# Kernel optimization log

Hardware: AMD Instinct MI355X
Metric: run time of the kernel (lower is better)

## Reference

```python
import jax, jax.numpy as jnp
import numpy as np

N0, N1, N2, N3 = 600000, 100000, 10000, 1000
E0, E1, E2 = 1000000, 100000, 10000
DIN, DH, DOUT = 128, 256, 47


def _glorot(k, fan_in, fan_out):
    s = np.sqrt(2.0 / (fan_in + fan_out)).astype(np.float32)
    return jax.random.normal(k, (fan_in, fan_out), jnp.float32) * s


def setup_inputs() -> dict:
    key = jax.random.key(0)
    ks = jax.random.split(key, 13)
    return {
        "x": jax.random.normal(ks[0], (N0, DIN), jnp.float32),
        "src0": jax.random.randint(ks[1], (E0,), 0, N0, jnp.int32),
        "dst0": jax.random.randint(ks[2], (E0,), 0, N1, jnp.int32),
        "src1": jax.random.randint(ks[3], (E1,), 0, N1, jnp.int32),
        "dst1": jax.random.randint(ks[4], (E1,), 0, N2, jnp.int32),
        "src2": jax.random.randint(ks[5], (E2,), 0, N2, jnp.int32),
        "dst2": jax.random.randint(ks[6], (E2,), 0, N3, jnp.int32),
        "Wl0": _glorot(ks[7], DIN, DH), "Wr0": _glorot(ks[8], DIN, DH),
        "b0": jnp.zeros((DH,), jnp.float32),
        "Wl1": _glorot(ks[9], DH, DH), "Wr1": _glorot(ks[10], DH, DH),
        "b1": jnp.zeros((DH,), jnp.float32),
        "Wl2": _glorot(ks[11], DH, DOUT), "Wr2": _glorot(ks[12], DH, DOUT),
        "b2": jnp.zeros((DOUT,), jnp.float32),
        "size1": N1, "size2": N2, "size3": N3,
    }


def _sage_conv(x, src, dst, n_tgt, Wl, Wr, b):
    # PyG SAGEConv (mean aggr, root_weight=True, bias in lin_l) on a bipartite
    # sampled subgraph: x_src = x (all frontier nodes), x_tgt = x[:n_tgt].
    msgs = x[src]                                   # [E, Din] gather
    agg = jax.ops.segment_sum(msgs, dst, num_segments=n_tgt)
    cnt = jax.ops.segment_sum(jnp.ones((dst.shape[0],), x.dtype), dst,
                              num_segments=n_tgt)
    mean = agg / jnp.maximum(cnt, 1.0)[:, None]     # [n_tgt, Din]
    return mean @ Wl + b + x[:n_tgt] @ Wr           # [n_tgt, Dout]


def reference(x, src0, dst0, src1, dst1, src2, dst2,
              Wl0, Wr0, b0, Wl1, Wr1, b1, Wl2, Wr2, b2,
              size1, size2, size3):
    # layer 0
    h = jax.nn.relu(_sage_conv(x, src0, dst0, size1, Wl0, Wr0, b0))
    # dropout(p=0.5) is identity in eval mode
    # layer 1
    h = jax.nn.relu(_sage_conv(h, src1, dst1, size2, Wl1, Wr1, b1))
    # layer 2 (no relu/dropout)
    h = _sage_conv(h, src2, dst2, size3, Wl2, Wr2, b2)
    return jax.nn.log_softmax(h, axis=-1)           # [size3, out_channels]
```

## Files before the change

### kernel.cpp

```cpp
#include <hip/hip_runtime.h>
#include <hip/hip_bf16.h>
#include <cstdint>
#include <cstddef>
#include <cmath>

#define N0C 600000
#define N1C 100000
#define N2C 10000
#define N3C 1000
#define E0C 1000000
#define E1C 100000
#define E2C 10000

typedef unsigned short u16;
typedef unsigned int u32;
typedef __attribute__((ext_vector_type(8))) short bf16x8;
typedef __attribute__((ext_vector_type(4))) float f32x4;

__device__ __forceinline__ u16 f2b(float x) {
  u32 u = __builtin_bit_cast(u32, x);
  u32 r = (u + 0x7fffu + ((u >> 16) & 1u)) >> 16;
  return (u16)r;
}
__device__ __forceinline__ u16 f2b_hw(float x) {
  __hip_bfloat16 h = __float2bfloat16(x);
  u16 r;
  __builtin_memcpy(&r, &h, 2);
  return r;
}
__device__ __forceinline__ float b2f(u16 h) {
  u32 u = ((u32)h) << 16;
  return __builtin_bit_cast(float, u);
}

__global__ __launch_bounds__(256) void hist3(
    const int* __restrict__ d0, const int* __restrict__ d1,
    const int* __restrict__ d2, int* __restrict__ c0, int* __restrict__ c1,
    int* __restrict__ c2) {
  int i = blockIdx.x * blockDim.x + threadIdx.x;
  if (i < E0C) atomicAdd(&c0[d0[i]], 1);
  else if (i < E0C + E1C) atomicAdd(&c1[d1[i - E0C]], 1);
  else if (i < E0C + E1C + E2C) atomicAdd(&c2[d2[i - E0C - E1C]], 1);
}

__global__ __launch_bounds__(256) void scan_block3(
    int* __restrict__ c0, int* __restrict__ c1, int* __restrict__ c2,
    int* __restrict__ p0, int* __restrict__ p1, int* __restrict__ p2) {
  __shared__ int sdata[256];
  const int b = blockIdx.x;
  int* data; int n; int* partials; int lb;
  if (b < 98)       { data = c0; n = N1C; partials = p0; lb = b; }
  else if (b < 108) { data = c1; n = N2C; partials = p1; lb = b - 98; }
  else              { data = c2; n = N3C; partials = p2; lb = b - 108; }
  const int t = threadIdx.x;
  const int idx = lb * 1024 + t * 4;
  int v[4];
  int sum = 0;
#pragma unroll
  for (int k = 0; k < 4; k++) {
    int x = (idx + k < n) ? data[idx + k] : 0;
    v[k] = x; sum += x;
  }
  sdata[t] = sum;
  __syncthreads();
  for (int off = 1; off < 256; off <<= 1) {
    int x = (t >= off) ? sdata[t - off] : 0;
    __syncthreads();
    sdata[t] += x;
    __syncthreads();
  }
  int run = (t > 0) ? sdata[t - 1] : 0;
#pragma unroll
  for (int k = 0; k < 4; k++) {
    run += v[k];
    if (idx + k < n) data[idx + k] = run;
  }
  if (t == 255) partials[lb] = sdata[255];
}

__global__ __launch_bounds__(128) void scan_partials3(
    int* __restrict__ p0, int* __restrict__ p1, int* __restrict__ p2) {
  __shared__ int sdata[128];
  int* p; int nb;
  if (blockIdx.x == 0)      { p = p0; nb = 98; }
  else if (blockIdx.x == 1) { p = p1; nb = 10; }
  else                      { p = p2; nb = 1; }
  const int t = threadIdx.x;
  sdata[t] = (t < nb) ? p[t] : 0;
  __syncthreads();
  for (int off = 1; off < 128; off <<= 1) {
    int x = (t >= off) ? sdata[t - off] : 0;
    __syncthreads();
    sdata[t] += x;
    __syncthreads();
  }
  int ex = (t > 0) ? sdata[t - 1] : 0;
  if (t < nb) p[t] = ex;
}

__global__ __launch_bounds__(256) void addoff3(
    const int* __restrict__ c0, const int* __restrict__ c1,
    const int* __restrict__ c2, const int* __restrict__ p0,
    const int* __restrict__ p1, const int* __restrict__ p2,
    int* __restrict__ o0, int* __restrict__ o1, int* __restrict__ o2) {
  int i = blockIdx.x * blockDim.x + threadIdx.x;
  if (i < N1C) {
    o0[i + 1] = c0[i] + p0[i >> 10];
    if (i == 0) o0[0] = 0;
  } else if (i < N1C + N2C) {
    int j = i - N1C;
    o1[j + 1] = c1[j] + p1[j >> 10];
    if (j == 0) o1[0] = 0;
  } else if (i < N1C + N2C + N3C) {
    int j = i - N1C - N2C;
    o2[j + 1] = c2[j] + p2[j >> 10];
    if (j == 0) o2[0] = 0;
  }
}

__global__ __launch_bounds__(256) void fill3(
    const int* __restrict__ s0, const int* __restrict__ d0,
    const int* __restrict__ s1, const int* __restrict__ d1,
    const int* __restrict__ s2, const int* __restrict__ d2,
    const int* __restrict__ o0, const int* __restrict__ o1,
    const int* __restrict__ o2, int* __restrict__ u0, int* __restrict__ u1,
    int* __restrict__ u2, int* __restrict__ e0, int* __restrict__ e1,
    int* __restrict__ e2) {
  int i = blockIdx.x * blockDim.x + threadIdx.x;
  if (i < E0C) {
    int d = d0[i]; int p = atomicAdd(&u0[d], 1); e0[o0[d] + p] = s0[i];
  } else if (i < E0C + E1C) {
    int j = i - E0C;
    int d = d1[j]; int p = atomicAdd(&u1[d], 1); e1[o1[d] + p] = s1[j];
  } else if (i < E0C + E1C + E2C) {
    int j = i - E0C - E1C;
    int d = d2[j]; int p = atomicAdd(&u2[d], 1); e2[o2[d] + p] = s2[j];
  }
}

__global__ __launch_bounds__(256) void cvt_wt2(
    const float* __restrict__ Wl0, const float* __restrict__ Wr0,
    const float* __restrict__ Wl1, const float* __restrict__ Wr1,
    u16* __restrict__ Wt0, u16* __restrict__ Wt1) {
  int idx = blockIdx.x * blockDim.x + threadIdx.x;
  if (idx < 256 * 256) {
    int n = idx >> 8, k = idx & 255;
    float v = (k < 128) ? Wl0[(size_t)k * 256 + n] : Wr0[(size_t)(k - 128) * 256 + n];
    Wt0[idx] = f2b(v);
  } else if (idx < 256 * 256 + 256 * 512) {
    int j = idx - 256 * 256;
    int n = j >> 9, k = j & 511;
    float v = (k < 256) ? Wl1[(size_t)k * 256 + n] : Wr1[(size_t)(k - 256) * 256 + n];
    Wt1[j] = f2b(v);
  }
}

__global__ __launch_bounds__(256) void gather128_f32(
    const float* __restrict__ X, const int* __restrict__ off,
    const int* __restrict__ esrc, int Nt, u16* __restrict__ mean) {
  int w = (blockIdx.x * blockDim.x + threadIdx.x) >> 6;
  int lane = threadIdx.x & 63;
  if (w >= Nt) return;
  int s = off[w], e = off[w + 1];
  float a0 = 0.f, a1 = 0.f;
  int j = s;
  for (; j + 3 < e; j += 4) {
    float2 r0 = *(const float2*)(X + (size_t)esrc[j + 0] * 128 + lane * 2);
    float2 r1 = *(const float2*)(X + (size_t)esrc[j + 1] * 128 + lane * 2);
    float2 r2 = *(const float2*)(X + (size_t)esrc[j + 2] * 128 + lane * 2);
    float2 r3 = *(const float2*)(X + (size_t)esrc[j + 3] * 128 + lane * 2);
    a0 += r0.x + r1.x + r2.x + r3.x;
    a1 += r0.y + r1.y + r2.y + r3.y;
  }
  for (; j < e; j++) {
    float2 r = *(const float2*)(X + (size_t)esrc[j] * 128 + lane * 2);
    a0 += r.x;
    a1 += r.y;
  }
  float inv = 1.0f / fmaxf((float)(e - s), 1.0f);
  u32 p = ((u32)f2b(a1 * inv) << 16) | (u32)f2b(a0 * inv);
  ((u32*)(mean + (size_t)w * 128))[lane] = p;
}

__global__ __launch_bounds__(256) void gather256_bf16(
    const u16* __restrict__ X, const int* __restrict__ off,
    const int* __restrict__ esrc, int Nt, u16* __restrict__ mean) {
  int w = (blockIdx.x * blockDim.x + threadIdx.x) >> 6;
  int lane = threadIdx.x & 63;
  if (w >= Nt) return;
  int s = off[w], e = off[w + 1];
  float a0 = 0.f, a1 = 0.f, a2 = 0.f, a3 = 0.f;
  int j = s;
  for (; j + 3 < e; j += 4) {
    ushort4 v0 = *(const ushort4*)(X + (size_t)esrc[j + 0] * 256 + lane * 4);
    ushort4 v1 = *(const ushort4*)(X + (size_t)esrc[j + 1] * 256 + lane * 4);
    ushort4 v2 = *(const ushort4*)(X + (size_t)esrc[j + 2] * 256 + lane * 4);
    ushort4 v3 = *(const ushort4*)(X + (size_t)esrc[j + 3] * 256 + lane * 4);
    a0 += b2f(v0.x) + b2f(v1.x) + b2f(v2.x) + b2f(v3.x);
    a1 += b2f(v0.y) + b2f(v1.y) + b2f(v2.y) + b2f(v3.y);
    a2 += b2f(v0.z) + b2f(v1.z) + b2f(v2.z) + b2f(v3.z);
    a3 += b2f(v0.w) + b2f(v1.w) + b2f(v2.w) + b2f(v3.w);
  }
  for (; j < e; j++) {
    ushort4 v0 = *(const ushort4*)(X + (size_t)esrc[j] * 256 + lane * 4);
    a0 += b2f(v0.x); a1 += b2f(v0.y); a2 += b2f(v0.z); a3 += b2f(v0.w);
  }
  float inv = 1.0f / fmaxf((float)(e - s), 1.0f);
  ushort4 o;
  o.x = f2b(a0 * inv); o.y = f2b(a1 * inv); o.z = f2b(a2 * inv); o.w = f2b(a3 * inv);
  *(ushort4*)(mean + (size_t)w * 256 + lane * 4) = o;
}

__global__ __launch_bounds__(256) void gemm_mfma(
    const u16* __restrict__ A1, const u16* __restrict__ A2, int Kh,
    const u16* __restrict__ Wt, const float* __restrict__ bias,
    u16* __restrict__ C, int M, int do_relu) {
  const int tid = threadIdx.x;
  const int wave = tid >> 6, lane = tid & 63;
  const int lr = lane & 15, quad = lane >> 4;
  const int wr = wave >> 1, wc = wave & 1;
  const int rowBase = blockIdx.x * 128 + wr * 64;
  const int colBase = blockIdx.y * 128 + wc * 64;
  const int Ktot = 2 * Kh;

  f32x4 acc[4][4] = {};

  size_t aoff[4];
#pragma unroll
  for (int mt = 0; mt < 4; mt++) {
    int r = rowBase + mt * 16 + lr;
    if (r >= M) r = M - 1;
    aoff[mt] = (size_t)r * Kh;
  }
  const u16* wrow[4];
  float bs[4];
#pragma unroll
  for (int nt = 0; nt < 4; nt++) {
    int n = colBase + nt * 16 + lr;
    wrow[nt] = Wt + (size_t)n * Ktot;
    bs[nt] = bias[n];
  }

#pragma unroll
  for (int half = 0; half < 2; half++) {
    const u16* Asrc = half ? A2 : A1;
    const int kb = half * Kh;
    for (int kt = 0; kt < Kh; kt += 32) {
      bf16x8 af[4], bfr[4];
#pragma unroll
      for (int mt = 0; mt < 4; mt++)
        af[mt] = *(const bf16x8*)(Asrc + aoff[mt] + kt + quad * 8);
#pragma unroll
      for (int nt = 0; nt < 4; nt++)
        bfr[nt] = *(const bf16x8*)(wrow[nt] + kb + kt + quad * 8);
#pragma unroll
      for (int mt = 0; mt < 4; mt++)
#pragma unroll
        for (int nt = 0; nt < 4; nt++)
          acc[mt][nt] = __builtin_amdgcn_mfma_f32_16x16x32_bf16(
              af[mt], bfr[nt], acc[mt][nt], 0, 0, 0);
    }
  }

#pragma unroll
  for (int mt = 0; mt < 4; mt++) {
#pragma unroll
    for (int reg = 0; reg < 4; reg++) {
      int row = rowBase + mt * 16 + quad * 4 + reg;
      if (row < M) {
#pragma unroll
        for (int nt = 0; nt < 4; nt++) {
          float v = acc[mt][nt][reg] + bs[nt];
          if (do_relu) v = fmaxf(v, 0.f);
          C[(size_t)row * 256 + colBase + nt * 16 + lr] = f2b(v);
        }
      }
    }
  }
}

__global__ __launch_bounds__(256) void gemm_mfma_l0(
    const u16* __restrict__ A1, const float* __restrict__ A2,
    const u16* __restrict__ Wt, const float* __restrict__ bias,
    u16* __restrict__ C, int M) {
  const int tid = threadIdx.x;
  const int wave = tid >> 6, lane = tid & 63;
  const int lr = lane & 15, quad = lane >> 4;
  const int wr = wave >> 1, wc = wave & 1;
  const int rowBase = blockIdx.x * 128 + wr * 64;
  const int colBase = blockIdx.y * 128 + wc * 64;

  f32x4 acc[4][4] = {};

  int rrow[4];
#pragma unroll
  for (int mt = 0; mt < 4; mt++) {
    int r = rowBase + mt * 16 + lr;
    if (r >= M) r = M - 1;
    rrow[mt] = r;
  }
  const u16* wrow[4];
  float bs[4];
#pragma unroll
  for (int nt = 0; nt < 4; nt++) {
    int n = colBase + nt * 16 + lr;
    wrow[nt] = Wt + (size_t)n * 256;
    bs[nt] = bias[n];
  }

  for (int kt = 0; kt < 128; kt += 32) {
    bf16x8 af[4], bfr[4];
#pragma unroll
    for (int mt = 0; mt < 4; mt++)
      af[mt] = *(const bf16x8*)(A1 + (size_t)rrow[mt] * 128 + kt + quad * 8);
#pragma unroll
    for (int nt = 0; nt < 4; nt++)
      bfr[nt] = *(const bf16x8*)(wrow[nt] + kt + quad * 8);
#pragma unroll
    for (int mt = 0; mt < 4; mt++)
#pragma unroll
      for (int nt = 0; nt < 4; nt++)
        acc[mt][nt] = __builtin_amdgcn_mfma_f32_16x16x32_bf16(
            af[mt], bfr[nt], acc[mt][nt], 0, 0, 0);
  }
  for (int kt = 0; kt < 128; kt += 32) {
    bf16x8 af[4], bfr[4];
#pragma unroll
    for (int mt = 0; mt < 4; mt++) {
      const float* s = A2 + (size_t)rrow[mt] * 128 + kt + quad * 8;
      float4 v0 = *(const float4*)s;
      float4 v1 = *(const float4*)(s + 4);
      bf16x8 t;
      t[0] = (short)f2b_hw(v0.x); t[1] = (short)f2b_hw(v0.y);
      t[2] = (short)f2b_hw(v0.z); t[3] = (short)f2b_hw(v0.w);
      t[4] = (short)f2b_hw(v1.x); t[5] = (short)f2b_hw(v1.y);
      t[6] = (short)f2b_hw(v1.z); t[7] = (short)f2b_hw(v1.w);
      af[mt] = t;
    }
#pragma unroll
    for (int nt = 0; nt < 4; nt++)
      bfr[nt] = *(const bf16x8*)(wrow[nt] + 128 + kt + quad * 8);
#pragma unroll
    for (int mt = 0; mt < 4; mt++)
#pragma unroll
      for (int nt = 0; nt < 4; nt++)
        acc[mt][nt] = __builtin_amdgcn_mfma_f32_16x16x32_bf16(
            af[mt], bfr[nt], acc[mt][nt], 0, 0, 0);
  }

#pragma unroll
  for (int mt = 0; mt < 4; mt++) {
#pragma unroll
    for (int reg = 0; reg < 4; reg++) {
      int row = rowBase + mt * 16 + quad * 4 + reg;
      if (row < M) {
#pragma unroll
        for (int nt = 0; nt < 4; nt++) {
          float v = fmaxf(acc[mt][nt][reg] + bs[nt], 0.f);
          C[(size_t)row * 256 + colBase + nt * 16 + lr] = f2b(v);
        }
      }
    }
  }
}

__global__ __launch_bounds__(64) void layer2_lsm(
    const u16* __restrict__ mean2, const u16* __restrict__ h2,
    const float* __restrict__ Wl2, const float* __restrict__ Wr2,
    const float* __restrict__ b2, float* __restrict__ out) {
  __shared__ float arow[512];
  const int i = blockIdx.x;
  const int lane = threadIdx.x;
  for (int t = lane; t < 256; t += 64) {
    arow[t] = b2f(mean2[(size_t)i * 256 + t]);
    arow[256 + t] = b2f(h2[(size_t)i * 256 + t]);
  }
  __syncthreads();
  float acc = 0.0f;
  if (lane < 47) {
    acc = b2[lane];
#pragma unroll 4
    for (int k = 0; k < 256; k++) acc += arow[k] * Wl2[k * 47 + lane];
#pragma unroll 4
    for (int k = 0; k < 256; k++) acc += arow[256 + k] * Wr2[k * 47 + lane];
  }
  float v = (lane < 47) ? acc : -INFINITY;
#pragma unroll
  for (int off = 32; off >= 1; off >>= 1) v = fmaxf(v, __shfl_xor(v, off, 64));
  float e = (lane < 47) ? expf(acc - v) : 0.0f;
  float s = e;
#pragma unroll
  for (int off = 32; off >= 1; off >>= 1) s += __shfl_xor(s, off, 64);
  if (lane < 47) out[(size_t)i * 47 + lane] = acc - v - logf(s);
}

extern "C" void kernel_launch(void* const* d_in, const int* in_sizes, int n_in,
                              void* d_out, int out_size, void* d_ws, size_t ws_size,
                              hipStream_t stream) {
  (void)in_sizes; (void)n_in; (void)out_size; (void)ws_size;
  const float* x   = (const float*)d_in[0];
  const int* src0  = (const int*)d_in[1];
  const int* dst0  = (const int*)d_in[2];
  const int* src1  = (const int*)d_in[3];
  const int* dst1  = (const int*)d_in[4];
  const int* src2  = (const int*)d_in[5];
  const int* dst2  = (const int*)d_in[6];
  const float* Wl0 = (const float*)d_in[7];
  const float* Wr0 = (const float*)d_in[8];
  const float* b0  = (const float*)d_in[9];
  const float* Wl1 = (const float*)d_in[10];
  const float* Wr1 = (const float*)d_in[11];
  const float* b1  = (const float*)d_in[12];
  const float* Wl2 = (const float*)d_in[13];
  const float* Wr2 = (const float*)d_in[14];
  const float* b2  = (const float*)d_in[15];

  char* p = (char*)d_ws;
  u16* mean0 = (u16*)p; p += (size_t)N1C * 128 * 2;
  u16* h1    = (u16*)p; p += (size_t)N1C * 256 * 2;
  u16* mean1 = (u16*)p; p += (size_t)N2C * 256 * 2;
  u16* h2    = (u16*)p; p += (size_t)N2C * 256 * 2;
  u16* mean2 = (u16*)p; p += (size_t)N3C * 256 * 2;
  u16* Wt0   = (u16*)p; p += (size_t)256 * 256 * 2;
  u16* Wt1   = (u16*)p; p += (size_t)256 * 512 * 2;
  int* cnt0  = (int*)p;
  int* cur0  = cnt0 + 100000;
  int* cnt1  = cur0 + 100000;
  int* cur1  = cnt1 + 10000;
  int* cnt2  = cur1 + 10000;
  int* cur2  = cnt2 + 1000;
  int* off0  = cur2 + 1000 + 48;
  int* off1  = off0 + 100096;
  int* off2  = off1 + 10112;
  int* part0 = off2 + 1088;
  int* part1 = part0 + 128;
  int* part2 = part1 + 128;
  int* esrc0 = part2 + 128;
  int* esrc1 = esrc0 + 1000000;
  int* esrc2 = esrc1 + 100000;
  float* out = (float*)d_out;

  hipMemsetAsync(cnt0, 0, (size_t)222000 * 4, stream);
  hist3<<<(E0C + E1C + E2C + 255) / 256, 256, 0, stream>>>(
      dst0, dst1, dst2, cnt0, cnt1, cnt2);
  scan_block3<<<109, 256, 0, stream>>>(cnt0, cnt1, cnt2, part0, part1, part2);
  scan_partials3<<<3, 128, 0, stream>>>(part0, part1, part2);
  addoff3<<<(N1C + N2C + N3C + 255) / 256, 256, 0, stream>>>(
      cnt0, cnt1, cnt2, part0, part1, part2, off0, off1, off2);
  fill3<<<(E0C + E1C + E2C + 255) / 256, 256, 0, stream>>>(
      src0, dst0, src1, dst1, src2, dst2, off0, off1, off2,
      cur0, cur1, cur2, esrc0, esrc1, esrc2);

  cvt_wt2<<<(256 * 256 + 256 * 512 + 255) / 256, 256, 0, stream>>>(
      Wl0, Wr0, Wl1, Wr1, Wt0, Wt1);

  gather128_f32<<<N1C / 4, 256, 0, stream>>>(x, off0, esrc0, N1C, mean0);
  gemm_mfma_l0<<<dim3(782, 2), 256, 0, stream>>>(mean0, x, Wt0, b0, h1, N1C);

  gather256_bf16<<<N2C / 4, 256, 0, stream>>>(h1, off1, esrc1, N2C, mean1);
  gemm_mfma<<<dim3(79, 2), 256, 0, stream>>>(mean1, h1, 256, Wt1, b1, h2, N2C, 1);

  gather256_bf16<<<N3C / 4, 256, 0, stream>>>(h2, off2, esrc2, N3C, mean2);
  layer2_lsm<<<N3C, 64, 0, stream>>>(mean2, h2, Wl2, Wr2, b2, out);
}
```

Baseline: 745.3 us.

## Fuse layer-0 gather into GEMM via LDS and fuse layer-2 gather with output

```diff
diff --git a/kernel.cpp b/kernel.cpp
--- a/kernel.cpp
+++ b/kernel.cpp
@@ -153,33 +153,6 @@
     float v = (k < 256) ? Wl1[(size_t)k * 256 + n] : Wr1[(size_t)(k - 256) * 256 + n];
     Wt1[j] = f2b(v);
   }
-}
-
-__global__ __launch_bounds__(256) void gather128_f32(
-    const float* __restrict__ X, const int* __restrict__ off,
-    const int* __restrict__ esrc, int Nt, u16* __restrict__ mean) {
-  int w = (blockIdx.x * blockDim.x + threadIdx.x) >> 6;
-  int lane = threadIdx.x & 63;
-  if (w >= Nt) return;
-  int s = off[w], e = off[w + 1];
-  float a0 = 0.f, a1 = 0.f;
-  int j = s;
-  for (; j + 3 < e; j += 4) {
-    float2 r0 = *(const float2*)(X + (size_t)esrc[j + 0] * 128 + lane * 2);
-    float2 r1 = *(const float2*)(X + (size_t)esrc[j + 1] * 128 + lane * 2);
-    float2 r2 = *(const float2*)(X + (size_t)esrc[j + 2] * 128 + lane * 2);
-    float2 r3 = *(const float2*)(X + (size_t)esrc[j + 3] * 128 + lane * 2);
-    a0 += r0.x + r1.x + r2.x + r3.x;
-    a1 += r0.y + r1.y + r2.y + r3.y;
-  }
-  for (; j < e; j++) {
-    float2 r = *(const float2*)(X + (size_t)esrc[j] * 128 + lane * 2);
-    a0 += r.x;
-    a1 += r.y;
-  }
-  float inv = 1.0f / fmaxf((float)(e - s), 1.0f);
-  u32 p = ((u32)f2b(a1 * inv) << 16) | (u32)f2b(a0 * inv);
-  ((u32*)(mean + (size_t)w * 128))[lane] = p;
 }
 
 __global__ __launch_bounds__(256) void gather256_bf16(
@@ -211,91 +184,54 @@
   *(ushort4*)(mean + (size_t)w * 256 + lane * 4) = o;
 }
 
-__global__ __launch_bounds__(256) void gemm_mfma(
-    const u16* __restrict__ A1, const u16* __restrict__ A2, int Kh,
-    const u16* __restrict__ Wt, const float* __restrict__ bias,
-    u16* __restrict__ C, int M, int do_relu) {
+__global__ __launch_bounds__(512) void l0_fused(
+    const float* __restrict__ x, const int* __restrict__ off,
+    const int* __restrict__ esrc, const u16* __restrict__ Wt,
+    const float* __restrict__ bias, u16* __restrict__ C, int M) {
+  __shared__ u16 Al[128 * 128];
   const int tid = threadIdx.x;
   const int wave = tid >> 6, lane = tid & 63;
+  const int rowBlk = blockIdx.x * 128;
+
+  for (int i = 0; i < 16; i++) {
+    const int lrow = wave * 16 + i;
+    const int node = rowBlk + lrow;
+    float a0 = 0.f, a1 = 0.f;
+    float inv = 0.f;
+    if (node < M) {
+      int s = off[node], e = off[node + 1];
+      int j = s;
+      for (; j + 3 < e; j += 4) {
+        float2 r0 = *(const float2*)(x + (size_t)esrc[j + 0] * 128 + lane * 2);
+        float2 r1 = *(const float2*)(x + (size_t)esrc[j + 1] * 128 + lane * 2);
+        float2 r2 = *(const float2*)(x + (size_t)esrc[j + 2] * 128 + lane * 2);
+        float2 r3 = *(const float2*)(x + (size_t)esrc[j + 3] * 128 + lane * 2);
+        a0 += r0.x + r1.x + r2.x + r3.x;
+        a1 += r0.y + r1.y + r2.y + r3.y;
+      }
+      for (; j < e; j++) {
+        float2 r = *(const float2*)(x + (size_t)esrc[j] * 128 + lane * 2);
+        a0 += r.x; a1 += r.y;
+      }
+      inv = 1.0f / fmaxf((float)(e - s), 1.0f);
+    }
+    u32 pck = ((u32)f2b(a1 * inv) << 16) | (u32)f2b(a0 * inv);
+    int pc = (lane >> 2) ^ (lrow & 7);
+    ((u32*)Al)[lrow * 64 + pc * 4 + (lane & 3)] = pck;
+  }
+  __syncthreads();
+
   const int lr = lane & 15, quad = lane >> 4;
-  const int wr = wave >> 1, wc = wave & 1;
-  const int rowBase = blockIdx.x * 128 + wr * 64;
-  const int colBase = blockIdx.y * 128 + wc * 64;
-  const int Ktot = 2 * Kh;
+  const int wr = wave >> 2, wc = wave & 3;
+  const int colBase = wc * 64;
 
   f32x4 acc[4][4] = {};
 
-  size_t aoff[4];
+  int lrw[4], rrow[4];
 #pragma unroll
   for (int mt = 0; mt < 4; mt++) {
-    int r = rowBase + mt * 16 + lr;
-    if (r >= M) r = M - 1;
-    aoff[mt] = (size_t)r * Kh;
-  }
-  const u16* wrow[4];
-  float bs[4];
-#pragma unroll
-  for (int nt = 0; nt < 4; nt++) {
-    int n = colBase + nt * 16 + lr;
-    wrow[nt] = Wt + (size_t)n * Ktot;
-    bs[nt] = bias[n];
-  }
-
-#pragma unroll
-  for (int half = 0; half < 2; half++) {
-    const u16* Asrc = half ? A2 : A1;
-    const int kb = half * Kh;
-    for (int kt = 0; kt < Kh; kt += 32) {
-      bf16x8 af[4], bfr[4];
-#pragma unroll
-      for (int mt = 0; mt < 4; mt++)
-        af[mt] = *(const bf16x8*)(Asrc + aoff[mt] + kt + quad * 8);
-#pragma unroll
-      for (int nt = 0; nt < 4; nt++)
-        bfr[nt] = *(const bf16x8*)(wrow[nt] + kb + kt + quad * 8);
-#pragma unroll
-      for (int mt = 0; mt < 4; mt++)
-#pragma unroll
-        for (int nt = 0; nt < 4; nt++)
-          acc[mt][nt] = __builtin_amdgcn_mfma_f32_16x16x32_bf16(
-              af[mt], bfr[nt], acc[mt][nt], 0, 0, 0);
-    }
-  }
-
-#pragma unroll
-  for (int mt = 0; mt < 4; mt++) {
-#pragma unroll
-    for (int reg = 0; reg < 4; reg++) {
-      int row = rowBase + mt * 16 + quad * 4 + reg;
-      if (row < M) {
-#pragma unroll
-        for (int nt = 0; nt < 4; nt++) {
-          float v = acc[mt][nt][reg] + bs[nt];
-          if (do_relu) v = fmaxf(v, 0.f);
-          C[(size_t)row * 256 + colBase + nt * 16 + lr] = f2b(v);
-        }
-      }
-    }
-  }
-}
-
-__global__ __launch_bounds__(256) void gemm_mfma_l0(
-    const u16* __restrict__ A1, const float* __restrict__ A2,
-    const u16* __restrict__ Wt, const float* __restrict__ bias,
-    u16* __restrict__ C, int M) {
-  const int tid = threadIdx.x;
-  const int wave = tid >> 6, lane = tid & 63;
-  const int lr = lane & 15, quad = lane >> 4;
-  const int wr = wave >> 1, wc = wave & 1;
-  const int rowBase = blockIdx.x * 128 + wr * 64;
-  const int colBase = blockIdx.y * 128 + wc * 64;
-
-  f32x4 acc[4][4] = {};
-
-  int rrow[4];
-#pragma unroll
-  for (int mt = 0; mt < 4; mt++) {
-    int r = rowBase + mt * 16 + lr;
+    lrw[mt] = wr * 64 + mt * 16 + lr;
+    int r = rowBlk + lrw[mt];
     if (r >= M) r = M - 1;
     rrow[mt] = r;
   }
@@ -308,11 +244,15 @@
     bs[nt] = bias[n];
   }
 
+#pragma unroll
   for (int kt = 0; kt < 128; kt += 32) {
     bf16x8 af[4], bfr[4];
 #pragma unroll
-    for (int mt = 0; mt < 4; mt++)
-      af[mt] = *(const bf16x8*)(A1 + (size_t)rrow[mt] * 128 + kt + quad * 8);
+    for (int mt = 0; mt < 4; mt++) {
+      int r = lrw[mt];
+      int pc = ((kt >> 3) + quad) ^ (r & 7);
+      af[mt] = *(const bf16x8*)(Al + r * 128 + pc * 8);
+    }
 #pragma unroll
     for (int nt = 0; nt < 4; nt++)
       bfr[nt] = *(const bf16x8*)(wrow[nt] + kt + quad * 8);
@@ -323,11 +263,12 @@
         acc[mt][nt] = __builtin_amdgcn_mfma_f32_16x16x32_bf16(
             af[mt], bfr[nt], acc[mt][nt], 0, 0, 0);
   }
+#pragma unroll
   for (int kt = 0; kt < 128; kt += 32) {
     bf16x8 af[4], bfr[4];
 #pragma unroll
     for (int mt = 0; mt < 4; mt++) {
-      const float* s = A2 + (size_t)rrow[mt] * 128 + kt + quad * 8;
+      const float* s = x + (size_t)rrow[mt] * 128 + kt + quad * 8;
       float4 v0 = *(const float4*)s;
       float4 v1 = *(const float4*)(s + 4);
       bf16x8 t;
@@ -352,7 +293,7 @@
   for (int mt = 0; mt < 4; mt++) {
 #pragma unroll
     for (int reg = 0; reg < 4; reg++) {
-      int row = rowBase + mt * 16 + quad * 4 + reg;
+      int row = rowBlk + wr * 64 + mt * 16 + quad * 4 + reg;
       if (row < M) {
 #pragma unroll
         for (int nt = 0; nt < 4; nt++) {
@@ -364,18 +305,112 @@
   }
 }
 
-__global__ __launch_bounds__(64) void layer2_lsm(
-    const u16* __restrict__ mean2, const u16* __restrict__ h2,
-    const float* __restrict__ Wl2, const float* __restrict__ Wr2,
-    const float* __restrict__ b2, float* __restrict__ out) {
+__global__ __launch_bounds__(512) void gemm_mfma1(
+    const u16* __restrict__ A1, const u16* __restrict__ A2, int Kh,
+    const u16* __restrict__ Wt, const float* __restrict__ bias,
+    u16* __restrict__ C, int M, int do_relu) {
+  const int tid = threadIdx.x;
+  const int wave = tid >> 6, lane = tid & 63;
+  const int lr = lane & 15, quad = lane >> 4;
+  const int wr = wave >> 2, wc = wave & 3;
+  const int rowBase = blockIdx.x * 128 + wr * 64;
+  const int colBase = wc * 64;
+  const int Ktot = 2 * Kh;
+
+  f32x4 acc[4][4] = {};
+
+  size_t aoff[4];
+#pragma unroll
+  for (int mt = 0; mt < 4; mt++) {
+    int r = rowBase + mt * 16 + lr;
+    if (r >= M) r = M - 1;
+    aoff[mt] = (size_t)r * Kh;
+  }
+  const u16* wrow[4];
+  float bs[4];
+#pragma unroll
+  for (int nt = 0; nt < 4; nt++) {
+    int n = colBase + nt * 16 + lr;
+    wrow[nt] = Wt + (size_t)n * Ktot;
+    bs[nt] = bias[n];
+  }
+
+#pragma unroll
+  for (int half = 0; half < 2; half++) {
+    const u16* Asrc = half ? A2 : A1;
+    const int kb = half * Kh;
+    for (int kt = 0; kt < Kh; kt += 32) {
+      bf16x8 af[4], bfr[4];
+#pragma unroll
+      for (int mt = 0; mt < 4; mt++)
+        af[mt] = *(const bf16x8*)(Asrc + aoff[mt] + kt + quad * 8);
+#pragma unroll
+      for (int nt = 0; nt < 4; nt++)
+        bfr[nt] = *(const bf16x8*)(wrow[nt] + kb + kt + quad * 8);
+#pragma unroll
+      for (int mt = 0; mt < 4; mt++)
+#pragma unroll
+        for (int nt = 0; nt < 4; nt++)
+          acc[mt][nt] = __builtin_amdgcn_mfma_f32_16x16x32_bf16(
+              af[mt], bfr[nt], acc[mt][nt], 0, 0, 0);
+    }
+  }
+
+#pragma unroll
+  for (int mt = 0; mt < 4; mt++) {
+#pragma unroll
+    for (int reg = 0; reg < 4; reg++) {
+      int row = rowBase + mt * 16 + quad * 4 + reg;
+      if (row < M) {
+#pragma unroll
+        for (int nt = 0; nt < 4; nt++) {
+          float v = acc[mt][nt][reg] + bs[nt];
+          if (do_relu) v = fmaxf(v, 0.f);
+          C[(size_t)row * 256 + colBase + nt * 16 + lr] = f2b(v);
+        }
+      }
+    }
+  }
+}
+
+__global__ __launch_bounds__(64) void l2_fused(
+    const u16* __restrict__ h2, const int* __restrict__ off,
+    const int* __restrict__ esrc, const float* __restrict__ Wl2,
+    const float* __restrict__ Wr2, const float* __restrict__ b2,
+    float* __restrict__ out) {
   __shared__ float arow[512];
   const int i = blockIdx.x;
   const int lane = threadIdx.x;
-  for (int t = lane; t < 256; t += 64) {
-    arow[t] = b2f(mean2[(size_t)i * 256 + t]);
-    arow[256 + t] = b2f(h2[(size_t)i * 256 + t]);
-  }
+
+  int s = off[i], e = off[i + 1];
+  float a0 = 0.f, a1 = 0.f, a2 = 0.f, a3 = 0.f;
+  int j = s;
+  for (; j + 3 < e; j += 4) {
+    ushort4 v0 = *(const ushort4*)(h2 + (size_t)esrc[j + 0] * 256 + lane * 4);
+    ushort4 v1 = *(const ushort4*)(h2 + (size_t)esrc[j + 1] * 256 + lane * 4);
+    ushort4 v2 = *(const ushort4*)(h2 + (size_t)esrc[j + 2] * 256 + lane * 4);
+    ushort4 v3 = *(const ushort4*)(h2 + (size_t)esrc[j + 3] * 256 + lane * 4);
+    a0 += b2f(v0.x) + b2f(v1.x) + b2f(v2.x) + b2f(v3.x);
+    a1 += b2f(v0.y) + b2f(v1.y) + b2f(v2.y) + b2f(v3.y);
+    a2 += b2f(v0.z) + b2f(v1.z) + b2f(v2.z) + b2f(v3.z);
+    a3 += b2f(v0.w) + b2f(v1.w) + b2f(v2.w) + b2f(v3.w);
+  }
+  for (; j < e; j++) {
+    ushort4 v0 = *(const ushort4*)(h2 + (size_t)esrc[j] * 256 + lane * 4);
+    a0 += b2f(v0.x); a1 += b2f(v0.y); a2 += b2f(v0.z); a3 += b2f(v0.w);
+  }
+  float inv = 1.0f / fmaxf((float)(e - s), 1.0f);
+  arow[lane * 4 + 0] = a0 * inv;
+  arow[lane * 4 + 1] = a1 * inv;
+  arow[lane * 4 + 2] = a2 * inv;
+  arow[lane * 4 + 3] = a3 * inv;
+  ushort4 r = *(const ushort4*)(h2 + (size_t)i * 256 + lane * 4);
+  arow[256 + lane * 4 + 0] = b2f(r.x);
+  arow[256 + lane * 4 + 1] = b2f(r.y);
+  arow[256 + lane * 4 + 2] = b2f(r.z);
+  arow[256 + lane * 4 + 3] = b2f(r.w);
   __syncthreads();
+
   float acc = 0.0f;
   if (lane < 47) {
     acc = b2[lane];
@@ -386,12 +421,12 @@
   }
   float v = (lane < 47) ? acc : -INFINITY;
 #pragma unroll
-  for (int off = 32; off >= 1; off >>= 1) v = fmaxf(v, __shfl_xor(v, off, 64));
-  float e = (lane < 47) ? expf(acc - v) : 0.0f;
-  float s = e;
-#pragma unroll
-  for (int off = 32; off >= 1; off >>= 1) s += __shfl_xor(s, off, 64);
-  if (lane < 47) out[(size_t)i * 47 + lane] = acc - v - logf(s);
+  for (int off2 = 32; off2 >= 1; off2 >>= 1) v = fmaxf(v, __shfl_xor(v, off2, 64));
+  float e2 = (lane < 47) ? expf(acc - v) : 0.0f;
+  float s2 = e2;
+#pragma unroll
+  for (int off2 = 32; off2 >= 1; off2 >>= 1) s2 += __shfl_xor(s2, off2, 64);
+  if (lane < 47) out[(size_t)i * 47 + lane] = acc - v - logf(s2);
 }
 
 extern "C" void kernel_launch(void* const* d_in, const int* in_sizes, int n_in,
@@ -416,11 +451,9 @@
   const float* b2  = (const float*)d_in[15];
 
   char* p = (char*)d_ws;
-  u16* mean0 = (u16*)p; p += (size_t)N1C * 128 * 2;
   u16* h1    = (u16*)p; p += (size_t)N1C * 256 * 2;
   u16* mean1 = (u16*)p; p += (size_t)N2C * 256 * 2;
   u16* h2    = (u16*)p; p += (size_t)N2C * 256 * 2;
-  u16* mean2 = (u16*)p; p += (size_t)N3C * 256 * 2;
   u16* Wt0   = (u16*)p; p += (size_t)256 * 256 * 2;
   u16* Wt1   = (u16*)p; p += (size_t)256 * 512 * 2;
   int* cnt0  = (int*)p;
@@ -454,12 +487,10 @@
   cvt_wt2<<<(256 * 256 + 256 * 512 + 255) / 256, 256, 0, stream>>>(
       Wl0, Wr0, Wl1, Wr1, Wt0, Wt1);
 
-  gather128_f32<<<N1C / 4, 256, 0, stream>>>(x, off0, esrc0, N1C, mean0);
-  gemm_mfma_l0<<<dim3(782, 2), 256, 0, stream>>>(mean0, x, Wt0, b0, h1, N1C);
+  l0_fused<<<782, 512, 0, stream>>>(x, off0, esrc0, Wt0, b0, h1, N1C);
 
   gather256_bf16<<<N2C / 4, 256, 0, stream>>>(h1, off1, esrc1, N2C, mean1);
-  gemm_mfma<<<dim3(79, 2), 256, 0, stream>>>(mean1, h1, 256, Wt1, b1, h2, N2C, 1);
-
-  gather256_bf16<<<N3C / 4, 256, 0, stream>>>(h2, off2, esrc2, N3C, mean2);
-  layer2_lsm<<<N3C, 64, 0, stream>>>(mean2, h2, Wl2, Wr2, b2, out);
-}
+  gemm_mfma1<<<79, 512, 0, stream>>>(mean1, h1, 256, Wt1, b1, h2, N2C, 1);
+
+  l2_fused<<<N3C, 64, 0, stream>>>(h2, off2, esrc2, Wl2, Wr2, b2, out);
+}
```

After: 897.8 us. 1.2x slower.
